# Kernel tuning notes

Measured on AMD Instinct MI355X. Metric: run time of the kernel, lower is better.

Reference implementation:

```python
import jax, jax.numpy as jnp
import numpy as np

TOPK = 13
NUM_CLASSES = 80
ALPHA = 1.0
BETA = 3.0
EPS = 1e-9
K_NEAR = 4
N_BINS = 36  # theta bins: arange(0, 360, 10)


def _dist_max_per_bin(anc_points, gt_pts):
    """gt_pts: (bs,nm,360,2), anc_points: (na,2) -> (bs,nm,na,36) ray targets."""
    d = gt_pts[:, :, None, :, :] - anc_points[None, None, :, None, :]  # (bs,nm,na,360,2)
    dist = jnp.sqrt(jnp.sum(d * d, axis=-1))                           # (bs,nm,na,360)
    ang = jnp.rad2deg(jnp.arctan2(d[..., 1], d[..., 0])) % 360.0       # (bs,nm,na,360)
    theta = jnp.arange(0, 360, 360 // N_BINS).astype(ang.dtype)        # (36,)

    def per_theta(th):
        diff = jnp.abs(ang - th)
        diff = jnp.where(diff > 180.0, 360.0 - diff, diff)
        neg_v, idx = jax.lax.top_k(-diff, K_NEAR)   # 4 nearest-angle contour pts
        val = -neg_v
        dk = jnp.take_along_axis(dist, idx, axis=-1)
        dk = jnp.where(jnp.min(val, axis=-1, keepdims=True) > 3.0, 1e-6, dk)
        return jnp.max(dk, axis=-1)                 # (bs,nm,na)

    dm = jax.lax.map(per_theta, theta)              # (36,bs,nm,na); chunked to bound memory
    return jnp.maximum(jnp.moveaxis(dm, 0, -1), 1e-6)


def _mask_iou(target, pred):
    l_max = jnp.maximum(target, pred)
    l_min = jnp.maximum(jnp.minimum(target, pred), 1e-6)
    return jnp.sum(l_min, -1) / jnp.sum(l_max, -1)


def _forward(pd_scores, pd_bboxes, anc_points, gt_labels, gt_bboxes, mask_gt, gt_coor):
    bs, na, nc = pd_scores.shape
    nm = gt_bboxes.shape[1]
    gl = gt_labels[..., 0]            # (bs,nm) int
    mgt = mask_gt[..., 0]             # (bs,nm) float
    gt_pts = gt_coor.reshape(bs, nm, 360, 2)

    # select_candidates_in_gts: anchor center strictly inside gt box
    lt, rb = gt_bboxes[..., :2], gt_bboxes[..., 2:]
    deltas = jnp.concatenate([anc_points[None, None] - lt[:, :, None],
                              rb[:, :, None] - anc_points[None, None]], axis=-1)
    mask_in_gts = (jnp.min(deltas, -1) > 1e-9).astype(pd_scores.dtype)  # (bs,nm,na)
    mask_sel = (mask_in_gts * mgt[:, :, None]) > 0

    # get_box_metrics_polar (dense over (bs,nm,na) instead of boolean-mask select)
    dist_max = _dist_max_per_bin(anc_points, gt_pts)                    # (bs,nm,na,36)
    overlaps = jnp.where(mask_sel, _mask_iou(dist_max, pd_bboxes[:, None]), 0.0)
    bbox_scores = jnp.take_along_axis(jnp.swapaxes(pd_scores, 1, 2), gl[:, :, None], axis=1)
    bbox_scores = jnp.where(mask_sel, bbox_scores, 0.0)
    align_metric = (bbox_scores ** ALPHA) * (overlaps ** BETA)

    # select_topk_candidates
    _, topk_idxs = jax.lax.top_k(align_metric, TOPK)
    topk_idxs = jnp.where(mgt[:, :, None] > 0, topk_idxs, 0)
    count = jnp.sum(jax.nn.one_hot(topk_idxs, na, dtype=align_metric.dtype), axis=-2)
    mask_topk = jnp.where(count > 1, 0.0, count)
    mask_pos = mask_topk * mask_in_gts * mgt[:, :, None]

    # select_highest_overlaps
    fg = jnp.sum(mask_pos, -2)                                          # (bs,na)
    multi = fg[:, None, :] > 1
    is_max = jnp.moveaxis(jax.nn.one_hot(jnp.argmax(overlaps, 1), nm, dtype=mask_pos.dtype), -1, 1)
    mask_pos = jnp.where(multi, is_max, mask_pos)
    fg_mask = jnp.sum(mask_pos, -2)
    target_gt_idx = jnp.argmax(mask_pos, -2)                            # (bs,na)

    # per-positive ray-distance targets + polar centerness (dense, masked)
    mask_pos_b = mask_pos > 0
    gt_dist = jnp.where(mask_pos_b[..., None], dist_max, 0.0)           # (bs,nm,na,36)
    cent = jnp.sqrt(jnp.min(dist_max, -1) / jnp.max(dist_max, -1))
    centerness_gt = jnp.where(mask_pos_b, cent, 0.0)                    # (bs,nm,na)

    # get_targets
    target_labels = jnp.maximum(jnp.take_along_axis(gl, target_gt_idx, axis=1), 0)
    target_bboxes = jnp.take_along_axis(gt_bboxes, target_gt_idx[..., None], axis=1)
    target_scores = jax.nn.one_hot(target_labels, NUM_CLASSES, dtype=pd_scores.dtype)
    target_scores = jnp.where((fg_mask > 0)[..., None], target_scores, 0.0)

    am = align_metric * mask_pos
    pos_align = jnp.max(am, -1, keepdims=True)
    pos_ov = jnp.max(overlaps * mask_pos, -1, keepdims=True)
    norm_align = jnp.max(am * pos_ov / (pos_align + EPS), -2)[..., None]  # (bs,na,1)
    target_scores = target_scores * norm_align

    return (target_labels, target_bboxes, target_scores, mask_pos_b,
            target_gt_idx, gt_dist, centerness_gt, fg_mask > 0)


def setup_inputs():
    key = jax.random.key(0)
    k = jax.random.split(key, 6)
    bs, nc, nm = 2, 80, 10
    pts, strs = [], []
    for s in (8, 16, 32):  # 640x640 YOLO grid -> 8400 anchors
        n = 640 // s
        yv, xv = np.meshgrid(np.arange(n), np.arange(n), indexing='ij')
        pts.append(np.stack([(xv + 0.5) * s, (yv + 0.5) * s], -1).reshape(-1, 2))
        strs.append(np.full((pts[-1].shape[0], 1), s, dtype=np.float32))
    anc_points = jnp.asarray(np.concatenate(pts).astype(np.float32))
    stride_tensor = jnp.asarray(np.concatenate(strs))
    na = anc_points.shape[0]
    pd_scores = jax.random.uniform(k[0], (bs, na, nc), dtype=jnp.float32)
    pd_bboxes = jax.random.uniform(k[1], (bs, na, 36), dtype=jnp.float32) * 100.0 + 1.0
    gt_labels = jax.random.randint(k[2], (bs, nm, 1), 0, nc)
    ctr = jax.random.uniform(k[3], (bs, nm, 2), dtype=jnp.float32) * 440.0 + 100.0
    wh = jax.random.uniform(k[4], (bs, nm, 2), dtype=jnp.float32) * 140.0 + 40.0
    gt_bboxes = jnp.concatenate([ctr - wh / 2.0, ctr + wh / 2.0], -1)
    th = jnp.arange(360.0) * (jnp.pi / 180.0)
    rad = (jnp.min(wh, -1, keepdims=True) / 2.0) * (0.6 + 0.4 * jax.random.uniform(k[5], (bs, nm, 360), dtype=jnp.float32))
    ray = jnp.stack([jnp.cos(th), jnp.sin(th)], -1)  # (360,2)
    gt_coor = (ctr[:, :, None, :] + rad[..., None] * ray[None, None]).reshape(bs, nm, 720)
    mask_gt = jnp.ones((bs, nm, 1), dtype=jnp.float32).at[1, 7:].set(0.0)
    return dict(pd_scores=pd_scores, pd_bboxes=pd_bboxes, anc_points=anc_points,
                gt_labels=gt_labels, gt_bboxes=gt_bboxes, mask_gt=mask_gt,
                gt_coor=gt_coor, stride_tensor=stride_tensor, ss=640,
                gt_center=ctr, imgsz=640)


def reference(pd_scores, pd_bboxes, anc_points, gt_labels, gt_bboxes, mask_gt, gt_coor, stride_tensor, ss, gt_center, imgsz):
    # ss, gt_center, imgsz, stride_tensor are accepted (as in the torch signature) but unused
    return _forward(pd_scores, pd_bboxes, anc_points, gt_labels, gt_bboxes, mask_gt, gt_coor)
```

## Files before the change

### kernel.cpp

```cpp
#include <hip/hip_runtime.h>

#define BS 2
#define NM 10
#define NA 8400
#define NC 80
#define NBIN 36
#define KTOP 13
#define NRECT (BS*NM*3)
#define WDIST_CAP 16384

typedef unsigned long long ull;

__device__ __forceinline__ void rect_one(int bm, int lv,
    const float* __restrict__ gtb, const float* __restrict__ mgt,
    int& x0, int& y0, int& cx, int& cy, int& cnt, int& n, int& base){
  cnt = 0; x0 = 0; y0 = 0; cx = 0; cy = 0; n = 0; base = 0;
  if (mgt[bm] > 0.f){
    float s = (float)(8 << lv);
    n = 640 >> (3 + lv);
    base = (lv == 0) ? 0 : ((lv == 1) ? 6400 : 8000);
    float lx = gtb[bm*4+0], ly = gtb[bm*4+1];
    float rx = gtb[bm*4+2], ry = gtb[bm*4+3];
    int a0 = (int)ceilf(lx/s - 0.5f); a0 = min(max(a0, 0), n);
    while (a0 > 0   &&  (((a0-1)+0.5f)*s - lx > 1e-9f)) a0--;
    while (a0 < n   && !(((a0  )+0.5f)*s - lx > 1e-9f)) a0++;
    int a1 = (int)floorf(rx/s - 0.5f); a1 = min(max(a1, -1), n-1);
    while (a1 < n-1 &&  (rx - ((a1+1)+0.5f)*s > 1e-9f)) a1++;
    while (a1 >= 0  && !(rx - ((a1  )+0.5f)*s > 1e-9f)) a1--;
    int b0 = (int)ceilf(ly/s - 0.5f); b0 = min(max(b0, 0), n);
    while (b0 > 0   &&  (((b0-1)+0.5f)*s - ly > 1e-9f)) b0--;
    while (b0 < n   && !(((b0  )+0.5f)*s - ly > 1e-9f)) b0++;
    int b1 = (int)floorf(ry/s - 0.5f); b1 = min(max(b1, -1), n-1);
    while (b1 < n-1 &&  (ry - ((b1+1)+0.5f)*s > 1e-9f)) b1++;
    while (b1 >= 0  && !(ry - ((b1  )+0.5f)*s > 1e-9f)) b1--;
    cx = max(0, a1 - a0 + 1);
    cy = max(0, b1 - b0 + 1);
    cnt = cx * cy;
    x0 = a0; y0 = b0;
  }
}

__device__ __forceinline__ void rect_setup(int tid,
    const float* __restrict__ gtb, const float* __restrict__ mgt,
    int* sx0, int* sy0, int* scx, int* scy, int* scum, int* sn, int* sbase){
  if (tid < NRECT){
    int bm = tid/3, lv = tid - bm*3;
    int x0, y0, cx, cy, cnt, n, base;
    rect_one(bm, lv, gtb, mgt, x0, y0, cx, cy, cnt, n, base);
    sx0[tid] = x0; sy0[tid] = y0; scx[tid] = cx; scy[tid] = cy;
    scum[tid] = cnt; sn[tid] = n; sbase[tid] = base;
  }
  __syncthreads();
  if (tid < 64){
    int c = (tid < NRECT) ? scum[tid] : 0;
    int incl = c;
#pragma unroll
    for (int st = 1; st < 64; st <<= 1){
      int o = __shfl_up(incl, st);
      if (tid >= st) incl += o;
    }
    if (tid < NRECT) scum[tid] = incl - c;
    if (tid == NRECT-1) scum[NRECT] = incl;
  }
  __syncthreads();
}

__device__ __forceinline__ int pair_from_p(int p,
    const int* sx0, const int* sy0, const int* scx,
    const int* scum, const int* sn, const int* sbase){
  int lo = 0, hi = NRECT - 1;
  while (lo < hi){ int mid = (lo + hi + 1) >> 1; if (scum[mid] <= p) lo = mid; else hi = mid - 1; }
  int r = lo;
  int idx = p - scum[r];
  int cx = scx[r];
  int yi = idx / cx;
  int xi = idx - yi*cx;
  int a = sbase[r] + (sy0[r] + yi)*sn[r] + (sx0[r] + xi);
  int bm = r/3;
  return bm*NA + a;
}

__device__ __forceinline__ ull shflx_u64(ull v, int off){
  unsigned lo = (unsigned)v, hi = (unsigned)(v >> 32);
  lo = __shfl_xor(lo, off); hi = __shfl_xor(hi, off);
  return ((ull)hi << 32) | lo;
}

__global__ __launch_bounds__(128)
void k_dist(const float* __restrict__ pds, const float* __restrict__ pdb,
            const float* __restrict__ anc, const int* __restrict__ gl,
            const float* __restrict__ gtb, const float* __restrict__ mgt,
            const float* __restrict__ coor,
            float* __restrict__ out, float* __restrict__ wf){
  float* o_labels  = out;
  float* o_bboxes  = o_labels + BS*NA;
  float* o_scores  = o_bboxes + BS*NA*4;
  float* o_maskpos = o_scores + (size_t)BS*NA*NC;
  float* o_gtidx   = o_maskpos + BS*NM*NA;
  float* o_gtdist  = o_gtidx + BS*NA;
  float* o_cent    = o_gtdist + (size_t)BS*NM*NA*NBIN;
  float* o_fg      = o_cent + BS*NM*NA;

  float* w_align = wf + 16;
  float* w_ovl   = w_align + BS*NM*NA;
  float* w_dist  = w_ovl + BS*NM*NA;

  __shared__ int sx0[NRECT], sy0[NRECT], scx[NRECT], scy[NRECT], scum[NRECT+1], sn[NRECT], sbase[NRECT];
  __shared__ float4 s_ad[360];
  __shared__ int s_cnt[NBIN], s_off[NBIN+1], s_cur[NBIN];
  __shared__ float s_res[NBIN];
  __shared__ int s_fbl[NBIN];
  __shared__ int s_nfb;

  int tid = threadIdx.x;
  int lane = tid & 63, wave = tid >> 6;

  rect_setup(tid, gtb, mgt, sx0, sy0, scx, scy, scum, sn, sbase);
  int total = scum[NRECT];

  {
    int gtid = blockIdx.x*128 + tid, gsz = gridDim.x*128;
    float4 z4 = make_float4(0.f,0.f,0.f,0.f);
    float4* zs = (float4*)o_scores;
    for (int i = gtid; i < (BS*NA*NC)/4; i += gsz) zs[i] = z4;
    float4* zg = (float4*)o_gtdist;
    for (int i = gtid; i < (BS*NM*NA*NBIN)/4; i += gsz) zg[i] = z4;
    float4* zc = (float4*)o_cent;
    for (int i = gtid; i < (BS*NM*NA)/4; i += gsz) zc[i] = z4;
    float4* zm = (float4*)o_maskpos;
    for (int i = gtid; i < (BS*NM*NA)/4; i += gsz) zm[i] = z4;
    if (gtid < 16) wf[gtid] = 0.f;
    for (int t = gtid; t < BS*NA; t += gsz){
      int b = t / NA;
      o_gtidx[t] = 0.f;
      o_fg[t] = 0.f;
      int lbl = gl[b*NM]; if (lbl < 0) lbl = 0;
      o_labels[t] = (float)lbl;
      const float* bx = gtb + (b*NM)*4;
      ((float4*)o_bboxes)[t] = make_float4(bx[0], bx[1], bx[2], bx[3]);
    }
    for (int row = gtid; row < BS*NM*NA; row += gsz){
      int bm = row / NA;
      int a  = row - bm*NA;
      int lv = (a < 6400) ? 0 : ((a < 8000) ? 1 : 2);
      int ai = a - ((lv == 0) ? 0 : ((lv == 1) ? 6400 : 8000));
      int r = bm*3 + lv;
      bool inrect = false;
      if (scx[r] > 0 && scy[r] > 0){
        int n = sn[r];
        int y = ai / n, x = ai - y*n;
        inrect = (x >= sx0[r] && x < sx0[r]+scx[r] &&
                  y >= sy0[r] && y < sy0[r]+scy[r]);
      }
      if (!inrect) w_ovl[row] = 0.f;
    }
  }

  if (tid < NBIN) s_cnt[tid] = 0;
  if (tid == 0) s_nfb = 0;
  __syncthreads();

  int bin2 = tid >> 1;
  int slot2 = tid & 1;

  for (int p = blockIdx.x; p < total; p += gridDim.x){
    int t = pair_from_p(p, sx0, sy0, scx, scum, sn, sbase);
    int a = t % NA; int bm = t / NA; int b = bm / NM;
    float ax = anc[2*a], ay = anc[2*a+1];
    const float2* cc2 = (const float2*)(coor + bm*720);

    float pr = 0.f, sc = 0.f;
    if (wave == 0){
      if (lane < NBIN) pr = pdb[((size_t)b*NA + a)*NBIN + lane];
      int cls = gl[bm];
      sc = pds[((size_t)b*NA + a)*NC + cls];
    }

    float anR[3], diR[3]; int buR[3];
#pragma unroll
    for (int r = 0; r < 3; r++){
      int i = tid + r*128;
      buR[r] = -1;
      if (i < 360){
        float2 cxy = cc2[i];
        float dx = cxy.x - ax;
        float dy = cxy.y - ay;
        diR[r] = sqrtf(dx*dx + dy*dy);
        float an = atan2f(dy, dx) * 57.29577951308232f;
        if (an < 0.f) an += 360.f;
        anR[r] = an;
        int bu = min((int)(an * 0.1f), NBIN-1);
        buR[r] = bu;
        atomicAdd(&s_cnt[bu], 1);
      }
    }
    __syncthreads();

    if (wave == 0){
      int c = (lane < NBIN) ? s_cnt[lane] : 0;
      int incl = c;
#pragma unroll
      for (int st = 1; st < 64; st <<= 1){
        int o = __shfl_up(incl, st);
        if (lane >= st) incl += o;
      }
      if (lane < NBIN){ s_off[lane+1] = incl; s_cur[lane] = incl - c; }
      if (lane == 0) s_off[0] = 0;
    }
    __syncthreads();

    if (tid < NBIN) s_cnt[tid] = 0;
#pragma unroll
    for (int r = 0; r < 3; r++){
      if (buR[r] >= 0){
        int pos = atomicAdd(&s_cur[buR[r]], 1);
        s_ad[pos] = make_float4(anR[r], diR[r], (float)(tid + r*128), 0.f);
      }
    }
    __syncthreads();

#define EVALJ(J, TH) { \
      float4 ad = s_ad[J]; \
      unsigned int ixv = (unsigned int)(int)ad.z; \
      float df = fabsf(ad.x - (TH)); \
      df = fminf(df, 360.f - df); \
      ull key = ((ull)__float_as_uint(df) << 32) | ixv; \
      if (key < k3){ \
        k3 = key; d3 = ad.y; \
        if (k3 < k2){ ull tk=k2; k2=k3; k3=tk; float td=d2; d2=d3; d3=td; } \
        if (k2 < k1){ ull tk=k1; k1=k2; k2=tk; float td=d1; d1=d2; d2=td; } \
        if (k1 < k0){ ull tk=k0; k0=k1; k1=tk; float td=d0; d0=d1; d1=td; } \
      } }

    if (bin2 < NBIN){
      float th = (float)(bin2*10);
      int r0s, r0e, r1s, r1e;
      if (bin2 == 0)      { r0s = s_off[35]; r0e = s_off[36]; r1s = 0; r1e = s_off[2]; }
      else if (bin2 == 35){ r0s = s_off[34]; r0e = s_off[36]; r1s = 0; r1e = s_off[1]; }
      else                { r0s = s_off[bin2-1]; r0e = s_off[bin2+2]; r1s = 0; r1e = 0; }
      int L0 = r0e - r0s, L = L0 + (r1e - r1s);
      ull k0,k1,k2,k3; float d0,d1,d2,d3;
      k0=k1=k2=k3=~0ull; d0=d1=d2=d3=0.f;
      for (int w = slot2; w < L; w += 2){
        int j = (w < L0) ? (r0s + w) : (r1s + w - L0);
        EVALJ(j, th)
      }
      float v0m = 0.f, d4v = 0.f, dmax = 0.f;
#pragma unroll
      for (int r = 0; r < 4; r++){
        ull mk = k0; float md = d0;
        ull ok = shflx_u64(mk, 1); float od = __shfl_xor(md, 1);
        if (ok < mk){ mk = ok; md = od; }
        if (r == 0) v0m = __uint_as_float((unsigned)(mk >> 32));
        if (r == 3) d4v = __uint_as_float((unsigned)(mk >> 32));
        dmax = fmaxf(dmax, md);
        if (k0 == mk){ k0=k1; d0=d1; k1=k2; d1=d2; k2=k3; d2=d3; k3=~0ull; d3=0.f; }
      }
      if (slot2 == 0){
        if (!(v0m <= 3.0f)){
          s_res[bin2] = 1e-6f;
        } else if (!(d4v <= 9.99f)){
          int fi = atomicAdd(&s_nfb, 1);
          s_fbl[fi] = bin2;
        } else {
          s_res[bin2] = fmaxf(dmax, 1e-6f);
        }
      }
    }
    __syncthreads();

    if (wave == 0){
      int nfb = s_nfb;
      for (int f = 0; f < nfb; f++){
        int fb = s_fbl[f];
        float th = (float)(fb*10);
        ull k0,k1,k2,k3; float d0,d1,d2,d3;
        k0=k1=k2=k3=~0ull; d0=d1=d2=d3=0.f;
        for (int j = lane; j < 360; j += 64){
          EVALJ(j, th)
        }
        ull hk = k0; float hd = d0; int hp = 0;
        float dmax = 0.f;
#pragma unroll
        for (int r = 0; r < 4; r++){
          ull mk = hk; float md = hd;
#pragma unroll
          for (int off = 1; off < 64; off <<= 1){
            ull ok = shflx_u64(mk, off);
            float od = __shfl_xor(md, off);
            if (ok < mk){ mk = ok; md = od; }
          }
          if (hk == mk){
            hp++;
            hk = (hp==1)? k1 : (hp==2)? k2 : (hp==3)? k3 : ~0ull;
            hd = (hp==1)? d1 : (hp==2)? d2 : (hp==3)? d3 : 0.f;
          }
          dmax = fmaxf(dmax, md);
        }
        if (lane == 0) s_res[fb] = fmaxf(dmax, 1e-6f);
      }
      if (lane == 0) s_nfb = 0;

      float sum_min = 0.f, sum_max = 0.f;
      if (lane < NBIN){
        float dfin = s_res[lane];
        if (p < WDIST_CAP) w_dist[(size_t)p*NBIN + lane] = dfin;
        sum_max = fmaxf(dfin, pr);
        sum_min = fmaxf(fminf(dfin, pr), 1e-6f);
      }
      for (int off = 32; off > 0; off >>= 1){
        sum_min += __shfl_down(sum_min, off);
        sum_max += __shfl_down(sum_max, off);
      }
      if (lane == 0){
        float ov = sum_min / sum_max;
        w_align[t] = sc * ov * ov * ov;
        w_ovl[t]   = ov;
      }
    }
#undef EVALJ
    __syncthreads();
  }
}

__global__ __launch_bounds__(256)
void k_tail(const float* __restrict__ gtb, const float* __restrict__ mgt,
            const float* __restrict__ w_align, const float* __restrict__ w_ovl,
            const float* __restrict__ w_dist, const int* __restrict__ gl,
            float* __restrict__ o_labels, float* __restrict__ o_bboxes,
            float* __restrict__ o_maskpos, float* __restrict__ o_gtidx,
            float* __restrict__ o_fg,
            float* __restrict__ o_gtdist, float* __restrict__ o_cent,
            float* __restrict__ o_scores,
            int* __restrict__ w_sel, int* __restrict__ done){
  __shared__ int sx0[NRECT], sy0[NRECT], scx[NRECT], scy[NRECT], scum[NRECT+1], sn[NRECT], sbase[NRECT];
  __shared__ float sv[256*KTOP];
  __shared__ int   si[256*KTOP];
  __shared__ float wv4[4];
  __shared__ int   wi4[4];
  __shared__ int   sel[BS*NM*KTOP];
  __shared__ unsigned paB[BS*NM], poB[BS*NM];
  __shared__ int fcnt;
  __shared__ int   fT[BS*NM*KTOP];
  __shared__ int   fA[BS*NM*KTOP];
  __shared__ int   fL[BS*NM*KTOP];
  __shared__ float fV[BS*NM*KTOP];
  __shared__ int sLast;

  int tid = threadIdx.x;
  int lane = tid & 63, wave = tid >> 6;

  rect_setup(tid, gtb, mgt, sx0, sy0, scx, scy, scum, sn, sbase);

  int bm = blockIdx.x;
  {
    const float* al = w_align + (size_t)bm*NA;
    int pbase = scum[bm*3], pm1 = scum[bm*3+1], pm2 = scum[bm*3+2], pend = scum[bm*3+3];

    float v[KTOP]; int ix[KTOP];
#pragma unroll
    for (int j = 0; j < KTOP; j++){ v[j] = -1.f; ix[j] = 0x7fffffff; }
    for (int p = pbase + tid; p < pend; p += 256){
      int r = bm*3 + ((p >= pm1) + (p >= pm2));
      int idx = p - scum[r];
      int cx = scx[r];
      int yi = idx / cx;
      int xi = idx - yi*cx;
      int a = sbase[r] + (sy0[r] + yi)*sn[r] + (sx0[r] + xi);
      float x = al[a];
      if (x > v[KTOP-1]){
        v[KTOP-1] = x; ix[KTOP-1] = a;
#pragma unroll
        for (int j = KTOP-1; j > 0; j--){
          if (v[j] > v[j-1]){
            float tv = v[j-1]; v[j-1] = v[j]; v[j] = tv;
            int   ti = ix[j-1]; ix[j-1] = ix[j]; ix[j] = ti;
          }
        }
      }
    }
#pragma unroll
    for (int j = 0; j < KTOP; j++){ sv[tid*KTOP+j] = v[j]; si[tid*KTOP+j] = ix[j]; }

    int head = 0;
    for (int r = 0; r < KTOP; r++){
      float cv = sv[tid*KTOP + head];
      int   ci = si[tid*KTOP + head];
      float rv = cv; int ri = ci;
      for (int off = 32; off > 0; off >>= 1){
        float ov = __shfl_down(rv, off);
        int   oi = __shfl_down(ri, off);
        if (ov > rv || (ov == rv && oi < ri)){ rv = ov; ri = oi; }
      }
      if (lane == 0){ wv4[wave] = rv; wi4[wave] = ri; }
      __syncthreads();
      float Wv = wv4[0]; int Wi = wi4[0];
#pragma unroll
      for (int w = 1; w < 4; w++){
        float ov = wv4[w]; int oi = wi4[w];
        if (ov > Wv || (ov == Wv && oi < Wi)){ Wv = ov; Wi = oi; }
      }
      if (ci == Wi && head < KTOP-1) head++;
      if (tid == 0)
        __hip_atomic_store(&w_sel[bm*KTOP + r], (Wv > 0.f) ? Wi : -1,
                           __ATOMIC_RELAXED, __HIP_MEMORY_SCOPE_AGENT);
      __syncthreads();
    }
  }

  if (tid == 0){
    __threadfence();
    int old = __hip_atomic_fetch_add(done, 1, __ATOMIC_ACQ_REL, __HIP_MEMORY_SCOPE_AGENT);
    sLast = (old == BS*NM - 1) ? 1 : 0;
  }
  __syncthreads();
  if (!sLast) return;

  for (int s = tid; s < BS*NM*KTOP; s += 256)
    sel[s] = __hip_atomic_load(&w_sel[s], __ATOMIC_RELAXED, __HIP_MEMORY_SCOPE_AGENT);
  if (tid < BS*NM){ paB[tid] = 0u; poB[tid] = 0u; }
  if (tid == 0) fcnt = 0;
  __syncthreads();

  for (int s = tid; s < BS*NM*KTOP; s += 256){
    int a = sel[s];
    if (a >= 0){
      int sbm = s / KTOP;
      int b   = sbm / NM;
      int s0 = b*NM*KTOP;
      int cnt = 0, minS = 1 << 30;
      for (int s2 = s0; s2 < s0 + NM*KTOP; s2++){
        if (sel[s2] == a){ cnt++; if (s2 < minS) minS = s2; }
      }
      if (s == minS){
        int bi = sbm - b*NM;
        if (cnt > 1){
          float bv = -1.f; bi = 0;
#pragma unroll
          for (int mm = 0; mm < NM; mm++){
            float vv = w_ovl[((size_t)(b*NM+mm))*NA + a];
            if (vv > bv){ bv = vv; bi = mm; }
          }
        }
        int bmw = b*NM + bi;
        int ta  = b*NA + a;
        o_maskpos[(size_t)bmw*NA + a] = 1.f;
        o_gtidx[ta] = (float)bi;
        o_fg[ta] = 1.f;
        int lbl = gl[bmw]; if (lbl < 0) lbl = 0;
        o_labels[ta] = (float)lbl;
        const float* bx = gtb + bmw*4;
        ((float4*)o_bboxes)[ta] = make_float4(bx[0], bx[1], bx[2], bx[3]);
        float av  = w_align[(size_t)bmw*NA + a];
        float ovv = w_ovl[(size_t)bmw*NA + a];
        atomicMax(&paB[bmw], __float_as_uint(av));
        atomicMax(&poB[bmw], __float_as_uint(ovv));
        int j = atomicAdd(&fcnt, 1);
        fT[j] = bmw*NA + a; fA[j] = ta; fL[j] = lbl; fV[j] = av;
      }
    }
  }
  __syncthreads();

  int nf = fcnt;
  for (int j = tid; j < nf; j += 256){
    int tf = fT[j];
    int a = tf % NA; int bmw = tf / NA;
    int lv = (a < 6400) ? 0 : ((a < 8000) ? 1 : 2);
    int ai = a - ((lv == 0) ? 0 : ((lv == 1) ? 6400 : 8000));
    int r = bmw*3 + lv;
    int n = sn[r];
    int y = ai / n, x = ai - y*n;
    int p = scum[r] + (y - sy0[r])*scx[r] + (x - sx0[r]);
    const float4* src = (const float4*)(w_dist + (size_t)p*NBIN);
    float4* dst = (float4*)(o_gtdist + (size_t)tf*NBIN);
    float vmin = 1e30f, vmax = 0.f;
#pragma unroll
    for (int q = 0; q < 9; q++){
      float4 v4 = src[q];
      dst[q] = v4;
      vmin = fminf(vmin, fminf(fminf(v4.x, v4.y), fminf(v4.z, v4.w)));
      vmax = fmaxf(vmax, fmaxf(fmaxf(v4.x, v4.y), fmaxf(v4.z, v4.w)));
    }
    o_cent[tf] = sqrtf(vmin / vmax);
    float paf = __uint_as_float(paB[bmw]);
    float pof = __uint_as_float(poB[bmw]);
    o_scores[(size_t)fA[j]*NC + fL[j]] = fV[j] * pof / (paf + 1e-9f);
  }
}

extern "C" void kernel_launch(void* const* d_in, const int* in_sizes, int n_in,
                              void* d_out, int out_size, void* d_ws, size_t ws_size,
                              hipStream_t stream){
  const float* pds  = (const float*)d_in[0];
  const float* pdb  = (const float*)d_in[1];
  const float* anc  = (const float*)d_in[2];
  const int*   gl   = (const int*)  d_in[3];
  const float* gtb  = (const float*)d_in[4];
  const float* mgt  = (const float*)d_in[5];
  const float* coor = (const float*)d_in[6];

  float* out = (float*)d_out;
  float* o_labels  = out;
  float* o_bboxes  = o_labels + BS*NA;
  float* o_scores  = o_bboxes + BS*NA*4;
  float* o_maskpos = o_scores + (size_t)BS*NA*NC;
  float* o_gtidx   = o_maskpos + BS*NM*NA;
  float* o_gtdist  = o_gtidx + BS*NA;
  float* o_cent    = o_gtdist + (size_t)BS*NM*NA*NBIN;
  float* o_fg      = o_cent + BS*NM*NA;

  float* wf      = (float*)d_ws;
  int*   done    = (int*)d_ws;
  float* w_align = wf + 16;
  float* w_ovl   = w_align + BS*NM*NA;
  float* w_dist  = w_ovl + BS*NM*NA;
  int*   w_sel   = (int*)(w_dist + (size_t)WDIST_CAP*NBIN);

  k_dist<<<4608, 128, 0, stream>>>(pds, pdb, anc, gl, gtb, mgt, coor, out, wf);
  k_tail<<<BS*NM, 256, 0, stream>>>(gtb, mgt, w_align, w_ovl, w_dist, gl,
                                    o_labels, o_bboxes, o_maskpos, o_gtidx, o_fg,
                                    o_gtdist, o_cent, o_scores, w_sel, done);
}
```

Before: 155.9 us.

## Process two anchor-gt pairs per 256-thread block in distance kernel

Widens the k_dist block from 128 to 256 threads and has each 128-thread half handle its own (anchor, gt) pair, each with its own shared-memory buffers for binning, offsets and results. The grid drops from 4608 to 2400 blocks, and the per-pair work now runs in two halves at once. This is meant to amortise the block-wide syncs and the per-block rect setup over two pairs. The cost is that both halves wait at each block-wide barrier, so a half stuck in the fallback full scan stalls the other, and shared-memory use per block doubles.

Measured after the change: 160.3 us. +2.8%, slower.

```diff
diff --git a/kernel.cpp b/kernel.cpp
--- a/kernel.cpp
+++ b/kernel.cpp
@@ -86,7 +86,7 @@
   return ((ull)hi << 32) | lo;
 }
 
-__global__ __launch_bounds__(128)
+__global__ __launch_bounds__(256)
 void k_dist(const float* __restrict__ pds, const float* __restrict__ pdb,
             const float* __restrict__ anc, const int* __restrict__ gl,
             const float* __restrict__ gtb, const float* __restrict__ mgt,
@@ -106,20 +106,23 @@
   float* w_dist  = w_ovl + BS*NM*NA;
 
   __shared__ int sx0[NRECT], sy0[NRECT], scx[NRECT], scy[NRECT], scum[NRECT+1], sn[NRECT], sbase[NRECT];
-  __shared__ float4 s_ad[360];
-  __shared__ int s_cnt[NBIN], s_off[NBIN+1], s_cur[NBIN];
-  __shared__ float s_res[NBIN];
-  __shared__ int s_fbl[NBIN];
-  __shared__ int s_nfb;
+  __shared__ float4 s_ad[2][360];
+  __shared__ int s_cnt[2][NBIN], s_off[2][NBIN+1], s_cur[2][NBIN];
+  __shared__ float s_res[2][NBIN];
+  __shared__ int s_fbl[2][NBIN];
+  __shared__ int s_nfb[2];
 
   int tid = threadIdx.x;
-  int lane = tid & 63, wave = tid >> 6;
+  int h  = tid >> 7;
+  int ht = tid & 127;
+  int lane = ht & 63;
+  int wv = ht >> 6;
 
   rect_setup(tid, gtb, mgt, sx0, sy0, scx, scy, scum, sn, sbase);
   int total = scum[NRECT];
 
   {
-    int gtid = blockIdx.x*128 + tid, gsz = gridDim.x*128;
+    int gtid = blockIdx.x*256 + tid, gsz = gridDim.x*256;
     float4 z4 = make_float4(0.f,0.f,0.f,0.f);
     float4* zs = (float4*)o_scores;
     for (int i = gtid; i < (BS*NA*NC)/4; i += gsz) zs[i] = z4;
@@ -156,21 +159,28 @@
     }
   }
 
-  if (tid < NBIN) s_cnt[tid] = 0;
-  if (tid == 0) s_nfb = 0;
+  if (ht < NBIN) s_cnt[h][ht] = 0;
+  if (ht == 0) s_nfb[h] = 0;
   __syncthreads();
 
-  int bin2 = tid >> 1;
-  int slot2 = tid & 1;
-
-  for (int p = blockIdx.x; p < total; p += gridDim.x){
-    int t = pair_from_p(p, sx0, sy0, scx, scum, sn, sbase);
-    int a = t % NA; int bm = t / NA; int b = bm / NM;
-    float ax = anc[2*a], ay = anc[2*a+1];
-    const float2* cc2 = (const float2*)(coor + bm*720);
+  int bin2 = ht >> 1;
+  int slot2 = ht & 1;
+
+  for (int base = blockIdx.x*2; base < total; base += gridDim.x*2){
+    int p = base + h;
+    bool act = (p < total);
+    int t = 0, a = 0, bm = 0, b = 0;
+    float ax = 0.f, ay = 0.f;
+    const float2* cc2 = (const float2*)coor;
+    if (act){
+      t = pair_from_p(p, sx0, sy0, scx, scum, sn, sbase);
+      a = t % NA; bm = t / NA; b = bm / NM;
+      ax = anc[2*a]; ay = anc[2*a+1];
+      cc2 = (const float2*)(coor + bm*720);
+    }
 
     float pr = 0.f, sc = 0.f;
-    if (wave == 0){
+    if (act && wv == 0){
       if (lane < NBIN) pr = pdb[((size_t)b*NA + a)*NBIN + lane];
       int cls = gl[bm];
       sc = pds[((size_t)b*NA + a)*NC + cls];
@@ -179,9 +189,9 @@
     float anR[3], diR[3]; int buR[3];
 #pragma unroll
     for (int r = 0; r < 3; r++){
-      int i = tid + r*128;
+      int i = ht + r*128;
       buR[r] = -1;
-      if (i < 360){
+      if (act && i < 360){
         float2 cxy = cc2[i];
         float dx = cxy.x - ax;
         float dy = cxy.y - ay;
@@ -191,36 +201,36 @@
         anR[r] = an;
         int bu = min((int)(an * 0.1f), NBIN-1);
         buR[r] = bu;
-        atomicAdd(&s_cnt[bu], 1);
+        atomicAdd(&s_cnt[h][bu], 1);
       }
     }
     __syncthreads();
 
-    if (wave == 0){
-      int c = (lane < NBIN) ? s_cnt[lane] : 0;
+    if (wv == 0){
+      int c = (lane < NBIN) ? s_cnt[h][lane] : 0;
       int incl = c;
 #pragma unroll
       for (int st = 1; st < 64; st <<= 1){
         int o = __shfl_up(incl, st);
         if (lane >= st) incl += o;
       }
-      if (lane < NBIN){ s_off[lane+1] = incl; s_cur[lane] = incl - c; }
-      if (lane == 0) s_off[0] = 0;
+      if (lane < NBIN){ s_off[h][lane+1] = incl; s_cur[h][lane] = incl - c; }
+      if (lane == 0) s_off[h][0] = 0;
     }
     __syncthreads();
 
-    if (tid < NBIN) s_cnt[tid] = 0;
+    if (ht < NBIN) s_cnt[h][ht] = 0;
 #pragma unroll
     for (int r = 0; r < 3; r++){
       if (buR[r] >= 0){
-        int pos = atomicAdd(&s_cur[buR[r]], 1);
-        s_ad[pos] = make_float4(anR[r], diR[r], (float)(tid + r*128), 0.f);
+        int pos = atomicAdd(&s_cur[h][buR[r]], 1);
+        s_ad[h][pos] = make_float4(anR[r], diR[r], (float)(ht + r*128), 0.f);
       }
     }
     __syncthreads();
 
 #define EVALJ(J, TH) { \
-      float4 ad = s_ad[J]; \
+      float4 ad = s_ad[h][J]; \
       unsigned int ixv = (unsigned int)(int)ad.z; \
       float df = fabsf(ad.x - (TH)); \
       df = fminf(df, 360.f - df); \
@@ -232,12 +242,12 @@
         if (k1 < k0){ ull tk=k0; k0=k1; k1=tk; float td=d0; d0=d1; d1=td; } \
       } }
 
-    if (bin2 < NBIN){
+    if (act && bin2 < NBIN){
       float th = (float)(bin2*10);
       int r0s, r0e, r1s, r1e;
-      if (bin2 == 0)      { r0s = s_off[35]; r0e = s_off[36]; r1s = 0; r1e = s_off[2]; }
-      else if (bin2 == 35){ r0s = s_off[34]; r0e = s_off[36]; r1s = 0; r1e = s_off[1]; }
-      else                { r0s = s_off[bin2-1]; r0e = s_off[bin2+2]; r1s = 0; r1e = 0; }
+      if (bin2 == 0)      { r0s = s_off[h][35]; r0e = s_off[h][36]; r1s = 0; r1e = s_off[h][2]; }
+      else if (bin2 == 35){ r0s = s_off[h][34]; r0e = s_off[h][36]; r1s = 0; r1e = s_off[h][1]; }
+      else                { r0s = s_off[h][bin2-1]; r0e = s_off[h][bin2+2]; r1s = 0; r1e = 0; }
       int L0 = r0e - r0s, L = L0 + (r1e - r1s);
       ull k0,k1,k2,k3; float d0,d1,d2,d3;
       k0=k1=k2=k3=~0ull; d0=d1=d2=d3=0.f;
@@ -258,21 +268,21 @@
       }
       if (slot2 == 0){
         if (!(v0m <= 3.0f)){
-          s_res[bin2] = 1e-6f;
+          s_res[h][bin2] = 1e-6f;
         } else if (!(d4v <= 9.99f)){
-          int fi = atomicAdd(&s_nfb, 1);
-          s_fbl[fi] = bin2;
+          int fi = atomicAdd(&s_nfb[h], 1);
+          s_fbl[h][fi] = bin2;
         } else {
-          s_res[bin2] = fmaxf(dmax, 1e-6f);
+          s_res[h][bin2] = fmaxf(dmax, 1e-6f);
         }
       }
     }
     __syncthreads();
 
-    if (wave == 0){
-      int nfb = s_nfb;
+    if (wv == 0){
+      int nfb = act ? s_nfb[h] : 0;
       for (int f = 0; f < nfb; f++){
-        int fb = s_fbl[f];
+        int fb = s_fbl[h][f];
         float th = (float)(fb*10);
         ull k0,k1,k2,k3; float d0,d1,d2,d3;
         k0=k1=k2=k3=~0ull; d0=d1=d2=d3=0.f;
@@ -297,25 +307,27 @@
           }
           dmax = fmaxf(dmax, md);
         }
-        if (lane == 0) s_res[fb] = fmaxf(dmax, 1e-6f);
-      }
-      if (lane == 0) s_nfb = 0;
-
-      float sum_min = 0.f, sum_max = 0.f;
-      if (lane < NBIN){
-        float dfin = s_res[lane];
-        if (p < WDIST_CAP) w_dist[(size_t)p*NBIN + lane] = dfin;
-        sum_max = fmaxf(dfin, pr);
-        sum_min = fmaxf(fminf(dfin, pr), 1e-6f);
-      }
-      for (int off = 32; off > 0; off >>= 1){
-        sum_min += __shfl_down(sum_min, off);
-        sum_max += __shfl_down(sum_max, off);
-      }
-      if (lane == 0){
-        float ov = sum_min / sum_max;
-        w_align[t] = sc * ov * ov * ov;
-        w_ovl[t]   = ov;
+        if (lane == 0) s_res[h][fb] = fmaxf(dmax, 1e-6f);
+      }
+      if (lane == 0) s_nfb[h] = 0;
+
+      if (act){
+        float sum_min = 0.f, sum_max = 0.f;
+        if (lane < NBIN){
+          float dfin = s_res[h][lane];
+          if (p < WDIST_CAP) w_dist[(size_t)p*NBIN + lane] = dfin;
+          sum_max = fmaxf(dfin, pr);
+          sum_min = fmaxf(fminf(dfin, pr), 1e-6f);
+        }
+        for (int off = 32; off > 0; off >>= 1){
+          sum_min += __shfl_down(sum_min, off);
+          sum_max += __shfl_down(sum_max, off);
+        }
+        if (lane == 0){
+          float ov = sum_min / sum_max;
+          w_align[t] = sc * ov * ov * ov;
+          w_ovl[t]   = ov;
+        }
       }
     }
 #undef EVALJ
@@ -517,7 +529,7 @@
   float* w_dist  = w_ovl + BS*NM*NA;
   int*   w_sel   = (int*)(w_dist + (size_t)WDIST_CAP*NBIN);
 
-  k_dist<<<4608, 128, 0, stream>>>(pds, pdb, anc, gl, gtb, mgt, coor, out, wf);
+  k_dist<<<2400, 256, 0, stream>>>(pds, pdb, anc, gl, gtb, mgt, coor, out, wf);
   k_tail<<<BS*NM, 256, 0, stream>>>(gtb, mgt, w_align, w_ovl, w_dist, gl,
                                     o_labels, o_bboxes, o_maskpos, o_gtidx, o_fg,
                                     o_gtdist, o_cent, o_scores, w_sel, done);
```
